# Kernel tuning notes

Measured on AMD Instinct MI355X. Metric: run time of the kernel, lower is better.

## Reference

```python
import jax, jax.numpy as jnp
import numpy as np

K = 20
EPS = 1e-5

def _knn(x, k):
    # x: (B,C,N); returns indices of k nearest neighbors (incl. self): (B,N,k)
    xx = jnp.sum(x * x, axis=1)                          # (B,N)
    inner = jnp.einsum('bcn,bcm->bnm', x, x)             # (B,N,N)
    neg_d = 2.0 * inner - xx[:, :, None] - xx[:, None, :]
    return jax.lax.top_k(neg_d, k)[1]

def _graph_feature(x, k):
    # x: (B,C,N) -> (B,2C,N,k) with [x_j - x_i, x_i]
    idx = _knn(x, k)
    xt = jnp.transpose(x, (0, 2, 1))                     # (B,N,C)
    nb = jax.vmap(lambda f, i: f[i])(xt, idx)            # (B,N,k,C)
    ctr = xt[:, :, None, :]
    feat = jnp.concatenate([nb - ctr, jnp.broadcast_to(ctr, nb.shape)], axis=-1)
    return jnp.transpose(feat, (0, 3, 1, 2))

def _edge_block(h, w, g, b, k):
    # EdgeConv: graph feature -> 1x1 conv -> BN(eval, mean0/var1) -> LeakyReLU(0.2) -> max over k
    f = _graph_feature(h, k)
    f = jnp.einsum('oc,bcnk->bonk', w, f)
    f = g[None, :, None, None] * f / np.sqrt(1.0 + EPS) + b[None, :, None, None]
    f = jnp.where(f >= 0, f, 0.2 * f)
    return jnp.max(f, axis=-1)                           # (B,O,N)

def _forward(features_1, features_2, sw1, sg1, sb1, fw1, fg1, fb1, sw2, sg2, sb2, fw2, fg2, fb2, sw3, sg3, sb3, fw3, fg3, fb3, ew, eg, eb, att_w, tn_w, tn_wb, tn_bias, fc1_w, fc1_b, sc_w, sc_b):
    def dgcnn_pass(x):
        xyz = x[:, :3, :]
        sem = x[:, 3:, :]
        x1 = _edge_block(xyz, sw1, sg1, sb1, K)
        x2 = _edge_block(x1, sw2, sg2, sb2, K)
        x3 = _edge_block(x2, sw3, sg3, sb3, K)
        s1 = _edge_block(sem, fw1, fg1, fb1, K)
        s2 = _edge_block(s1, fw2, fg2, fb2, K)
        s3 = _edge_block(s2, fw3, fg3, fb3, K)
        h = jnp.concatenate([x3, s3], axis=1)            # (B,2*F3,N)
        h = jnp.einsum('oc,bcn->bon', ew, h)
        h = eg[None, :, None] * h / np.sqrt(1.0 + EPS) + eb[None, :, None]
        h = jnp.where(h >= 0, h, 0.2 * h)
        return jnp.transpose(h, (0, 2, 1))               # (B,N,F3)

    def attention(emb):
        gc = jnp.tanh(jnp.mean(jnp.einsum('bnf,fg->bng', emb, att_w), axis=1))  # (B,F)
        sc = jax.nn.sigmoid(jnp.einsum('bnf,bf->bn', emb, gc))[:, :, None]      # (B,N,1)
        pooled = jnp.einsum('bnf,bnk->bfk', emb, sc)                            # (B,F,1)
        return pooled, sc

    a1 = dgcnn_pass(features_1)
    a2 = dgcnn_pass(features_2)
    p1, att1 = attention(a1)
    p2, att2 = attention(a2)
    e1 = p1[:, :, 0]
    e2 = p2[:, :, 0]
    # NTN: e1^T W[:,:,t] e2 + V [e1;e2] + b
    scoring = jnp.einsum('bf,fgt,bg->bt', e1, tn_w, e2)
    block = jnp.einsum('tc,bc->bt', tn_wb, jnp.concatenate([e1, e2], axis=1))
    tscores = jax.nn.relu(scoring + block + tn_bias[:, 0][None, :])             # (B,T)
    h = jax.nn.relu(tscores @ fc1_w.T + fc1_b)
    score = jax.nn.sigmoid(h @ sc_w.T + sc_b).reshape(-1)                       # (B,)
    return score, att1, att2


def setup_inputs() -> dict:
    key = jax.random.key(0)
    ks = iter(jax.random.split(key, 40))
    def rn(shape, s=0.05):
        return jax.random.normal(next(ks), shape, dtype=jnp.float32) * s
    F1, F2, F3, T, BN = 64, 64, 128, 16, 16
    d = {}
    d['features_1'] = jax.random.normal(next(ks), (8, 131, 1024), dtype=jnp.float32)
    d['features_2'] = jax.random.normal(next(ks), (8, 131, 1024), dtype=jnp.float32)
    d['sw1'] = rn((F1, 6));        d['sg1'] = jnp.ones((F1,));  d['sb1'] = jnp.zeros((F1,))
    d['fw1'] = rn((F1, 256));      d['fg1'] = jnp.ones((F1,));  d['fb1'] = jnp.zeros((F1,))
    d['sw2'] = rn((F2, 2 * F1));   d['sg2'] = jnp.ones((F2,));  d['sb2'] = jnp.zeros((F2,))
    d['fw2'] = rn((F2, 2 * F1));   d['fg2'] = jnp.ones((F2,));  d['fb2'] = jnp.zeros((F2,))
    d['sw3'] = rn((F3, 2 * F2));   d['sg3'] = jnp.ones((F3,));  d['sb3'] = jnp.zeros((F3,))
    d['fw3'] = rn((F3, 2 * F2));   d['fg3'] = jnp.ones((F3,));  d['fb3'] = jnp.zeros((F3,))
    d['ew']  = rn((F3, 2 * F3));   d['eg']  = jnp.ones((F3,));  d['eb']  = jnp.zeros((F3,))
    d['att_w'] = rn((F3, F3))
    d['tn_w'] = rn((F3, F3, T))
    d['tn_wb'] = rn((T, 2 * F3))
    d['tn_bias'] = rn((T, 1))
    d['fc1_w'] = rn((BN, T));  d['fc1_b'] = jnp.zeros((BN,))
    d['sc_w'] = rn((1, BN));   d['sc_b'] = jnp.zeros((1,))
    return d


def reference(features_1, features_2, sw1, sg1, sb1, fw1, fg1, fb1, sw2, sg2, sb2, fw2, fg2, fb2, sw3, sg3, sb3, fw3, fg3, fb3, ew, eg, eb, att_w, tn_w, tn_wb, tn_bias, fc1_w, fc1_b, sc_w, sc_b):
    return _forward(features_1, features_2, sw1, sg1, sb1, fw1, fg1, fb1, sw2, sg2, sb2, fw2, fg2, fb2, sw3, sg3, sb3, fw3, fg3, fb3, ew, eg, eb, att_w, tn_w, tn_wb, tn_bias, fc1_w, fc1_b, sc_w, sc_b)
```

## Files before the change

kernel.cpp:

```cpp
#include <hip/hip_runtime.h>
#include <math.h>

#define INV_SQRT1P 0.99999500003749968754f

typedef short v8s  __attribute__((ext_vector_type(8)));
typedef float v16f __attribute__((ext_vector_type(16)));

static __device__ __forceinline__ float lrelu(float f){ return f >= 0.0f ? f : 0.2f*f; }

static __device__ __forceinline__ int lanecnt_below(unsigned long long m){
  int c = __builtin_amdgcn_mbcnt_lo((unsigned)m, 0u);
  return __builtin_amdgcn_mbcnt_hi((unsigned)(m >> 32), c);
}

__global__ void k_ext3(const float* __restrict__ f1, const float* __restrict__ f2,
                       float* __restrict__ out){
  int i = blockIdx.x*256 + threadIdx.x;
  int half = 8*3*1024;
  if (i >= 2*half) return;
  const float* f = (i < half) ? f1 : f2;
  int boff = (i < half) ? 0 : 8;
  int ii = (i < half) ? i : i - half;
  int n  = ii & 1023;
  int bc = ii >> 10;
  int c  = bc % 3;
  int b  = bc / 3;
  out[((size_t)(((b+boff)<<10)+n))*3 + c] = f[((size_t)(b*131 + c) << 10) + n];
}

__global__ __launch_bounds__(256) void k_extT(const float* __restrict__ f1,
    const float* __restrict__ f2, float* __restrict__ out){
  __shared__ float T[32][65];
  int bid = blockIdx.x;
  int nt = bid & 15;
  int ct = (bid >> 4) & 3;
  int bb = bid >> 6;
  const float* f = (bb < 8) ? f1 : f2;
  int b = bb & 7;
  int tid = threadIdx.x;
  #pragma unroll
  for (int it=0; it<8; it++){
    int cc = it*4 + (tid >> 6);
    int nn = tid & 63;
    T[cc][nn] = f[((size_t)(b*131 + 3 + ct*32 + cc) << 10) + nt*64 + nn];
  }
  __syncthreads();
  size_t rowb = ((size_t)bb << 10) + nt*64;
  #pragma unroll
  for (int it=0; it<8; it++){
    int nn = it*8 + (tid >> 5);
    int c  = tid & 31;
    out[(rowb + nn)*128 + ct*32 + c] = T[c][nn];
  }
}

__global__ __launch_bounds__(256) void k_pw(const float* __restrict__ X,
    unsigned short* __restrict__ PH, unsigned short* __restrict__ PL,
    float* __restrict__ xxout, const float* __restrict__ Wm,
    unsigned short* __restrict__ PWH, unsigned short* __restrict__ PWL,
    int C, int Kp, int O, int nwblk, int nrowsB, int wsplit, int doxx){
  int nkc = Kp >> 4;
  if ((int)blockIdx.x < nwblk){
    int gid = blockIdx.x*256 + threadIdx.x;
    int nchunk = (nrowsB/32)*nkc;
    if (gid >= nchunk*64) return;
    int lane = gid & 63;
    int chunk = gid >> 6;
    int jb = chunk / nkc, kc = chunk - jb*nkc;
    int j = jb*32 + (lane & 31);
    int k0 = kc*16 + ((lane>>5)<<3);
    unsigned short h[8], lo[8];
    #pragma unroll
    for (int t=0;t<8;t++){
      int k = k0 + t;
      float x = 0.f;
      if (k < C){
        if (wsplit) x = (j < O) ? Wm[(size_t)j*2*C + k] : Wm[(size_t)(j-O)*2*C + C + k];
        else        x = Wm[(size_t)j*C + k];
      }
      unsigned u = __float_as_uint(x);
      unsigned h16 = (u + 0x7fffu + ((u>>16)&1u)) >> 16;
      float hf = __uint_as_float(h16 << 16);
      float lf = x - hf;
      unsigned ul = __float_as_uint(lf);
      unsigned l16 = (ul + 0x7fffu + ((ul>>16)&1u)) >> 16;
      h[t] = (unsigned short)h16; lo[t] = (unsigned short)l16;
    }
    size_t o = (size_t)chunk*512 + lane*8;
    *(v8s*)(PWH + o) = *(v8s*)h;
    *(v8s*)(PWL + o) = *(v8s*)lo;
  } else {
    int gid = (blockIdx.x - nwblk)*256 + threadIdx.x;
    int lane = gid & 63;
    int chunk = gid >> 6;
    int rb = chunk / nkc, kc = chunk - rb*nkc;
    int row = rb*32 + (lane & 31);
    int k0 = kc*16 + ((lane>>5)<<3);
    unsigned short h[8], lo[8];
    const float* Xr = X + (size_t)row*C;
    #pragma unroll
    for (int j=0;j<8;j++){
      int k = k0 + j;
      float x = (k < C) ? Xr[k] : 0.f;
      unsigned u = __float_as_uint(x);
      unsigned h16 = (u + 0x7fffu + ((u>>16)&1u)) >> 16;
      float hf = __uint_as_float(h16 << 16);
      float lf = x - hf;
      unsigned ul = __float_as_uint(lf);
      unsigned l16 = (ul + 0x7fffu + ((ul>>16)&1u)) >> 16;
      h[j] = (unsigned short)h16; lo[j] = (unsigned short)l16;
    }
    size_t o = (size_t)chunk*512 + lane*8;
    *(v8s*)(PH + o) = *(v8s*)h;
    *(v8s*)(PL + o) = *(v8s*)lo;
    if (doxx && kc == 0 && (lane & 32) == 0){
      float s = 0.f;
      for (int c=0;c<C;c++) s += Xr[c]*Xr[c];
      xxout[row] = s;
    }
  }
}

__global__ __launch_bounds__(512) void k_dy(const unsigned short* __restrict__ PH,
    const unsigned short* __restrict__ PL, const unsigned short* __restrict__ PWH,
    const unsigned short* __restrict__ PWL, const float* __restrict__ xx,
    int* __restrict__ idx, float* __restrict__ Y, int Kp, int N, int npair, int nymf){
  __shared__ float Sl[16][1024];
  int wave = threadIdx.x >> 6;
  int l = threadIdx.x & 63;
  int nkc = Kp >> 4;

  if ((int)blockIdx.x < nymf){
    int gw = blockIdx.x*8 + wave;
    int mt = gw / npair;
    int pair = gw - mt*npair;
    int jb0 = pair*2, jb1 = pair*2 + 1;
    size_t ao  = ((size_t)mt*nkc)*512 + l*8;
    size_t b0o = ((size_t)jb0*nkc)*512 + l*8;
    size_t b1o = ((size_t)jb1*nkc)*512 + l*8;
    v16f acc0, acc1;
    #pragma unroll
    for (int i=0;i<16;i++){ acc0[i] = 0.f; acc1[i] = 0.f; }
    for (int kc=0; kc<nkc; kc++){
      v8s Ah  = *(const v8s*)(PH + ao);
      v8s Al  = *(const v8s*)(PL + ao);
      v8s B0h = *(const v8s*)(PWH + b0o);
      v8s B0l = *(const v8s*)(PWL + b0o);
      v8s B1h = *(const v8s*)(PWH + b1o);
      v8s B1l = *(const v8s*)(PWL + b1o);
      acc0 = __builtin_amdgcn_mfma_f32_32x32x16_bf16(Ah, B0h, acc0, 0, 0, 0);
      acc1 = __builtin_amdgcn_mfma_f32_32x32x16_bf16(Ah, B1h, acc1, 0, 0, 0);
      acc0 = __builtin_amdgcn_mfma_f32_32x32x16_bf16(Ah, B0l, acc0, 0, 0, 0);
      acc1 = __builtin_amdgcn_mfma_f32_32x32x16_bf16(Ah, B1l, acc1, 0, 0, 0);
      acc0 = __builtin_amdgcn_mfma_f32_32x32x16_bf16(Al, B0h, acc0, 0, 0, 0);
      acc1 = __builtin_amdgcn_mfma_f32_32x32x16_bf16(Al, B1h, acc1, 0, 0, 0);
      ao += 512; b0o += 512; b1o += 512;
    }
    int rbase = mt*32;
    int c0 = pair*64 + (l & 31), c1 = c0 + 32;
    #pragma unroll
    for (int r=0;r<16;r++){
      int rl_ = (r&3) + ((r>>2)<<3) + ((l>>5)<<2);
      float* dst = Y + (size_t)(rbase + rl_)*N;
      dst[c0] = acc0[r];
      dst[c1] = acc1[r];
    }
    return;
  }

  int t = blockIdx.x - nymf;
  int rb = ((t & 7) << 6) | (t >> 3);
  int batch = rb >> 5;
  const float* xxb = xx + (batch<<10);
  int rbase_local = (rb & 31)*32;

  v16f acc[4];
  #pragma unroll
  for (int i=0;i<4;i++){
    #pragma unroll
    for (int j=0;j<16;j++) acc[i][j] = 0.f;
  }
  #pragma unroll
  for (int pp=0; pp<2; pp++){
    int pair = wave*2 + pp;
    size_t a   = ((size_t)rb*nkc)*512 + l*8;
    size_t b0o = ((size_t)(batch*32 + 2*pair)*nkc)*512 + l*8;
    size_t b1o = b0o + (size_t)nkc*512;
    for (int kc=0; kc<nkc; kc++){
      v8s Ah  = *(const v8s*)(PH + a);
      v8s Al  = *(const v8s*)(PL + a);
      v8s B0h = *(const v8s*)(PH + b0o);
      v8s B0l = *(const v8s*)(PL + b0o);
      v8s B1h = *(const v8s*)(PH + b1o);
      v8s B1l = *(const v8s*)(PL + b1o);
      acc[2*pp]   = __builtin_amdgcn_mfma_f32_32x32x16_bf16(Ah, B0h, acc[2*pp],   0, 0, 0);
      acc[2*pp+1] = __builtin_amdgcn_mfma_f32_32x32x16_bf16(Ah, B1h, acc[2*pp+1], 0, 0, 0);
      acc[2*pp]   = __builtin_amdgcn_mfma_f32_32x32x16_bf16(Ah, B0l, acc[2*pp],   0, 0, 0);
      acc[2*pp+1] = __builtin_amdgcn_mfma_f32_32x32x16_bf16(Ah, B1l, acc[2*pp+1], 0, 0, 0);
      acc[2*pp]   = __builtin_amdgcn_mfma_f32_32x32x16_bf16(Al, B0h, acc[2*pp],   0, 0, 0);
      acc[2*pp+1] = __builtin_amdgcn_mfma_f32_32x32x16_bf16(Al, B1h, acc[2*pp+1], 0, 0, 0);
      a += 512; b0o += 512; b1o += 512;
    }
  }

  #pragma unroll
  for (int h=0; h<2; h++){
    #pragma unroll
    for (int pp=0; pp<2; pp++){
      int pair = wave*2 + pp;
      int c0 = pair*64 + (l & 31), c1 = c0 + 32;
      float xc0 = xxb[c0], xc1 = xxb[c1];
      #pragma unroll
      for (int r = 0; r < 8; r++){
        int rr = h*8 + r;
        int rl = (rr&3) + (((rr>>2)&1)<<3) + ((l>>5)<<2);
        float xr = xxb[rbase_local + h*16 + rl];
        Sl[rl][c0] = 2.f*acc[2*pp][rr]   - xr - xc0;
        Sl[rl][c1] = 2.f*acc[2*pp+1][rr] - xr - xc1;
      }
    }
    __syncthreads();
    {
      int hi = l >> 5;
      int li = l & 31;
      int rloc = wave*2 + hi;
      int grow = rb*32 + h*16 + rloc;
      int out_base = grow*20;
      unsigned long long hm = hi ? 0xFFFFFFFF00000000ull : 0x00000000FFFFFFFFull;

      unsigned kv[32];
      #pragma unroll
      for (int j=0;j<32;j++){
        unsigned u = __float_as_uint(Sl[rloc][li + 32*j]);
        kv[j] = (u & 0x80000000u) ? ~u : (u | 0x80000000u);
      }

      unsigned lmax = kv[0];
      #pragma unroll
      for (int j=1;j<32;j++) lmax = lmax > kv[j] ? lmax : kv[j];

      unsigned tau = 0u;
      #pragma unroll
      for (int bit=31; bit>=0; --bit){
        unsigned cand = tau | (1u << bit);
        unsigned long long M = __ballot(lmax >= cand);
        int c = hi ? __popc((unsigned)(M >> 32)) : __popc((unsigned)M);
        tau = (c >= 20) ? cand : tau;
      }

      unsigned long long* sl = (unsigned long long*)&Sl[rloc][0];
      sl[li] = 0ull; sl[li+32] = 0ull;
      int b2 = 0;
      #pragma unroll
      for (int j=0;j<32;j++){
        bool p = kv[j] >= tau;
        unsigned long long M = __ballot(p) & hm;
        if (p){
          int s = b2 + lanecnt_below(M);
          if (s < 64) sl[s] = ((unsigned long long)kv[j] << 32) | (unsigned)(li + 32*j);
        }
        b2 += __popcll(M);
      }

      if (b2 <= 64){
        unsigned long long pk0 = sl[li], pk1 = sl[li+32];
        unsigned vcur = 0u;
        #pragma unroll
        for (int bit=31; bit>=0; --bit){
          unsigned long long cc = (unsigned long long)(vcur | (1u << bit)) << 32;
          unsigned long long B0 = __ballot(pk0 >= cc);
          unsigned long long B1 = __ballot(pk1 >= cc);
          int clo = __popc((unsigned)B0) + __popc((unsigned)B1);
          int chi = __popc((unsigned)(B0>>32)) + __popc((unsigned)(B1>>32));
          int c = hi ? chi : clo;
          vcur = (c >= 20) ? (vcur | (1u << bit)) : vcur;
        }
        unsigned k0 = (unsigned)(pk0 >> 32), k1 = (unsigned)(pk1 >> 32);
        unsigned long long G0 = __ballot(k0 > vcur) & hm;
        unsigned long long G1 = __ballot(k1 > vcur) & hm;
        int ng0 = __popcll(G0);
        int c1  = ng0 + __popcll(G1);
        if (k0 > vcur) idx[out_base + lanecnt_below(G0)] = (int)(pk0 & 0xffffffffu);
        if (k1 > vcur) idx[out_base + ng0 + lanecnt_below(G1)] = (int)(pk1 & 0xffffffffu);
        unsigned long long E0 = __ballot(k0 == vcur) & hm;
        unsigned long long E1 = __ballot(k1 == vcur) & hm;
        int ne0 = __popcll(E0);
        if (k0 == vcur){ int s = c1 + lanecnt_below(E0); if (s < 20) idx[out_base + s] = (int)(pk0 & 0xffffffffu); }
        if (k1 == vcur){ int s = c1 + ne0 + lanecnt_below(E1); if (s < 20) idx[out_base + s] = (int)(pk1 & 0xffffffffu); }
      } else {
        unsigned cur = 0u;
        #pragma unroll 1
        for (int bit=31; bit>=0; --bit){
          unsigned cand = cur | (1u << bit);
          int lc = 0;
          #pragma unroll
          for (int j=0;j<32;j++) lc += (kv[j] >= cand) ? 1 : 0;
          #pragma unroll
          for (int off=1; off<32; off<<=1) lc += __shfl_xor(lc, off, 64);
          cur = (lc >= 20) ? cand : cur;
        }
        int bse = 0;
        #pragma unroll 1
        for (int j=0;j<32;j++){
          unsigned long long Mg = __ballot(kv[j] > cur) & hm;
          if (kv[j] > cur){ int s = bse + lanecnt_below(Mg); idx[out_base + s] = li + 32*j; }
          bse += __popcll(Mg);
        }
        #pragma unroll 1
        for (int j=0;j<32;j++){
          unsigned long long Me = __ballot(kv[j] == cur) & hm;
          if (kv[j] == cur){ int s = bse + lanecnt_below(Me); if (s < 20) idx[out_base + s] = li + 32*j; }
          bse += __popcll(Me);
          if (bse >= 20) break;
        }
      }
    }
    __syncthreads();
  }
}

__global__ __launch_bounds__(256) void k_emb(const unsigned short* __restrict__ PH,
    const unsigned short* __restrict__ PL, const unsigned short* __restrict__ PWH,
    const unsigned short* __restrict__ PWL, const float* __restrict__ eg,
    const float* __restrict__ eb, float* __restrict__ EMB){
  int w = threadIdx.x >> 6;
  int l = threadIdx.x & 63;
  int gw = blockIdx.x*4 + w;
  int mt = gw >> 1, pair = gw & 1;
  const int nkc = 16;
  size_t ao  = ((size_t)mt*nkc)*512 + l*8;
  size_t b0o = ((size_t)(pair*2)*nkc)*512 + l*8;
  size_t b1o = b0o + (size_t)nkc*512;
  v16f acc0, acc1;
  #pragma unroll
  for (int i=0;i<16;i++){ acc0[i] = 0.f; acc1[i] = 0.f; }
  for (int kc=0; kc<nkc; kc++){
    v8s Ah  = *(const v8s*)(PH + ao);
    v8s Al  = *(const v8s*)(PL + ao);
    v8s B0h = *(const v8s*)(PWH + b0o);
    v8s B0l = *(const v8s*)(PWL + b0o);
    v8s B1h = *(const v8s*)(PWH + b1o);
    v8s B1l = *(const v8s*)(PWL + b1o);
    acc0 = __builtin_amdgcn_mfma_f32_32x32x16_bf16(Ah, B0h, acc0, 0, 0, 0);
    acc1 = __builtin_amdgcn_mfma_f32_32x32x16_bf16(Ah, B1h, acc1, 0, 0, 0);
    acc0 = __builtin_amdgcn_mfma_f32_32x32x16_bf16(Ah, B0l, acc0, 0, 0, 0);
    acc1 = __builtin_amdgcn_mfma_f32_32x32x16_bf16(Ah, B1l, acc1, 0, 0, 0);
    acc0 = __builtin_amdgcn_mfma_f32_32x32x16_bf16(Al, B0h, acc0, 0, 0, 0);
    acc1 = __builtin_amdgcn_mfma_f32_32x32x16_bf16(Al, B1h, acc1, 0, 0, 0);
    ao += 512; b0o += 512; b1o += 512;
  }
  int rbase = mt*32;
  int c0 = pair*64 + (l & 31), c1 = c0 + 32;
  float g0 = eg[c0]*INV_SQRT1P, g1 = eg[c1]*INV_SQRT1P;
  float bb0 = eb[c0], bb1 = eb[c1];
  #pragma unroll
  for (int r=0;r<16;r++){
    int rl_ = (r&3) + ((r>>2)<<3) + ((l>>5)<<2);
    float* dst = EMB + (size_t)(rbase + rl_)*128;
    dst[c0] = lrelu(g0*acc0[r] + bb0);
    dst[c1] = lrelu(g1*acc1[r] + bb1);
  }
}

__global__ __launch_bounds__(256) void k_edge(const float* __restrict__ Y, const int* __restrict__ idx,
    const float* __restrict__ g, const float* __restrict__ bias,
    float* __restrict__ out, int O, int ldo, int ooff){
  int rpb = 256/O;
  int rloc = threadIdx.x/O;
  int o = threadIdx.x - rloc*O;
  int row = blockIdx.x*rpb + rloc;
  int b = row >> 10;
  __shared__ int js[4][20];
  int nj = rpb*20;
  if (threadIdx.x < nj) js[threadIdx.x/20][threadIdx.x%20] = idx[(blockIdx.x*rpb)*20 + threadIdx.x];
  __syncthreads();
  int O2 = O*2;
  float y1c = Y[(size_t)row*O2 + o];
  float d   = Y[(size_t)row*O2 + O + o] - y1c;
  float sc  = g[o] * INV_SQRT1P;
  float bb  = bias[o];
  const float* Yb = Y + ((size_t)(b<<10))*O2;
  float best = -1e38f;
  #pragma unroll
  for (int k=0;k<20;k++){
    float f = sc * (Yb[(size_t)js[rloc][k]*O2 + o] + d) + bb;
    best = fmaxf(best, lrelu(f));
  }
  out[(size_t)row*ldo + ooff + o] = best;
}

__global__ __launch_bounds__(1024) void k_meangc(const float* __restrict__ emb,
     const float* __restrict__ att_w, float* __restrict__ gc){
  int b = blockIdx.x; int f = threadIdx.x & 127; int ny = threadIdx.x >> 7;
  const float* e = emb + ((size_t)(b<<10) + ny*128)*128 + f;
  float s = 0.f;
  for (int n=0;n<128;n++) s += e[n*128];
  __shared__ float red[8][128];
  __shared__ float mr[128];
  red[ny][f] = s;
  __syncthreads();
  if (ny == 0){
    float t = 0.f;
    #pragma unroll
    for (int i=0;i<8;i++) t += red[i][f];
    mr[f] = t * (1.0f/1024.0f);
  }
  __syncthreads();
  if (threadIdx.x < 128){
    int g = threadIdx.x;
    float s2 = 0.f;
    for (int ff=0; ff<128; ff++) s2 += mr[ff]*att_w[ff*128+g];
    gc[b*128+g] = tanhf(s2);
  }
}

__global__ __launch_bounds__(256) void k_sc(const float* __restrict__ emb, const float* __restrict__ gc,
     float* __restrict__ sc, float* __restrict__ attout){
  int wave = threadIdx.x >> 6;
  int l = threadIdx.x & 63;
  int row = blockIdx.x*4 + wave;
  int b = row >> 10;
  const float* e  = emb + (size_t)row*128;
  const float* gb = gc + b*128;
  float p = e[l]*gb[l] + e[l+64]*gb[l+64];
  #pragma unroll
  for (int off=32; off>0; off>>=1) p += __shfl_xor(p, off, 64);
  if (l == 0){
    float s = 1.0f/(1.0f + expf(-p));
    sc[row] = s;
    attout[row] = s;
  }
}

__global__ __launch_bounds__(1024) void k_pool(const float* __restrict__ emb, const float* __restrict__ sc,
     float* __restrict__ ep){
  int b = blockIdx.x; int f = threadIdx.x & 127; int ny = threadIdx.x >> 7;
  const float* e  = emb + ((size_t)(b<<10) + ny*128)*128 + f;
  const float* sb = sc + (b<<10) + ny*128;
  float s = 0.f;
  for (int n=0;n<128;n++) s += e[n*128]*sb[n];
  __shared__ float red[8][128];
  red[ny][f] = s;
  __syncthreads();
  if (ny == 0){
    float t = 0.f;
    #pragma unroll
    for (int i=0;i<8;i++) t += red[i][f];
    ep[b*128+f] = t;
  }
}

__global__ __launch_bounds__(256) void k_tnet(const float* __restrict__ e1, const float* __restrict__ e2,
    const float* __restrict__ tn_w, const float* __restrict__ tn_wb, const float* __restrict__ tn_bias,
    float* __restrict__ tsout){
  int b = blockIdx.x; int t = threadIdx.x; int tt = t & 15; int fs = t >> 4;
  __shared__ float E1[128], E2[128], red[16][17];
  if (t < 128){ E1[t] = e1[b*128+t]; E2[t] = e2[b*128+t]; }
  __syncthreads();
  float acc = 0.f;
  for (int f = fs*8; f < fs*8+8; f++){
    const float* tw = tn_w + f*128*16 + tt;
    float partial = 0.f;
    for (int g=0; g<128; g++) partial += E2[g]*tw[g*16];
    acc += E1[f]*partial;
  }
  red[fs][tt] = acc;
  __syncthreads();
  if (t < 16){
    float s = 0.f;
    #pragma unroll
    for (int i=0;i<16;i++) s += red[i][t];
    float acc2 = 0.f;
    for (int c=0;c<128;c++) acc2 += tn_wb[t*256+c]*E1[c] + tn_wb[t*256+128+c]*E2[c];
    float v = s + acc2 + tn_bias[t];
    tsout[b*16+t] = v > 0.f ? v : 0.f;
  }
}

__global__ __launch_bounds__(128) void k_score2(const float* __restrict__ ts,
   const float* __restrict__ fc1_w, const float* __restrict__ fc1_b,
   const float* __restrict__ sc_w, const float* __restrict__ sc_b, float* __restrict__ out){
  int t = threadIdx.x; int b = t >> 4, i = t & 15;
  __shared__ float h2[8][17];
  float a = 0.f;
  #pragma unroll
  for (int k=0;k<16;k++) a += ts[b*16+k]*fc1_w[i*16+k];
  a += fc1_b[i];
  h2[b][i] = a > 0.f ? a : 0.f;
  __syncthreads();
  if (t < 8){
    float s = 0.f;
    #pragma unroll
    for (int k=0;k<16;k++) s += h2[t][k]*sc_w[k];
    s += sc_b[0];
    out[t] = 1.0f/(1.0f + expf(-s));
  }
}

extern "C" void kernel_launch(void* const* d_in, const int* in_sizes, int n_in,
                              void* d_out, int out_size, void* d_ws, size_t ws_size,
                              hipStream_t stream){
  const float* f1  = (const float*)d_in[0];
  const float* f2  = (const float*)d_in[1];
  const float* sw1 = (const float*)d_in[2];  const float* sg1 = (const float*)d_in[3];  const float* sb1 = (const float*)d_in[4];
  const float* fw1 = (const float*)d_in[5];  const float* fg1 = (const float*)d_in[6];  const float* fb1 = (const float*)d_in[7];
  const float* sw2 = (const float*)d_in[8];  const float* sg2 = (const float*)d_in[9];  const float* sb2 = (const float*)d_in[10];
  const float* fw2 = (const float*)d_in[11]; const float* fg2 = (const float*)d_in[12]; const float* fb2 = (const float*)d_in[13];
  const float* sw3 = (const float*)d_in[14]; const float* sg3 = (const float*)d_in[15]; const float* sb3 = (const float*)d_in[16];
  const float* fw3 = (const float*)d_in[17]; const float* fg3 = (const float*)d_in[18]; const float* fb3 = (const float*)d_in[19];
  const float* ew  = (const float*)d_in[20]; const float* eg  = (const float*)d_in[21]; const float* eb  = (const float*)d_in[22];
  const float* att_w   = (const float*)d_in[23];
  const float* tn_w    = (const float*)d_in[24];
  const float* tn_wb   = (const float*)d_in[25];
  const float* tn_bias = (const float*)d_in[26];
  const float* fc1_w   = (const float*)d_in[27];
  const float* fc1_b   = (const float*)d_in[28];
  const float* sc_w    = (const float*)d_in[29];
  const float* sc_b    = (const float*)d_in[30];

  float* W    = (float*)d_ws;
  float* T0   = W;
  float* T1   = W + 2097152;
  float* X3S3 = W + 4194304;
  float* EMB  = W + 8388608;
  float* xx   = W + 10485760;
  float* gcb  = W + 10504192;
  float* scb  = W + 10506240;
  float* ep   = W + 10522624;
  float* tsb  = W + 10524672;
  int*   idxb = (int*)(W + 10524800);
  unsigned short* PH = (unsigned short*)(W + 10852480);
  unsigned short* PL = (unsigned short*)(W + 11901056);
  unsigned short* PWH = (unsigned short*)(W + 12949632);
  unsigned short* PWL = (unsigned short*)(W + 12966016);
  float* REG  = W + 12982400;
  unsigned short* PH2 = (unsigned short*)(W + 17176704);
  unsigned short* PL2 = (unsigned short*)(W + 19273856);

  (void)ws_size;
  float* out = (float*)d_out;

  auto edge = [&](const float* xin, int C, int O,
                  const float* w, const float* g, const float* bb,
                  float* xout, int ldo, int ooff){
    int Kp = (C + 15) & ~15;
    int nkc = Kp >> 4;
    int npair = 2*O/64;
    int nwblk = ((2*O/32)*nkc*64 + 255)/256;
    int nymf  = 64*npair;
    k_pw<<<nwblk + 128*nkc, 256, 0, stream>>>(xin, PH, PL, xx, w, PWH, PWL,
        C, Kp, O, nwblk, 2*O, 1, 1);
    k_dy<<<nymf + 512, 512, 0, stream>>>(PH, PL, PWH, PWL, xx, idxb, REG, Kp, 2*O, npair, nymf);
    k_edge<<<16384/(256/O), 256, 0, stream>>>(REG, idxb, g, bb, xout, O, ldo, ooff);
  };

  k_ext3<<<(2*8*3*1024+255)/256, 256, 0, stream>>>(f1, f2, T0);
  edge(T0, 3,   64, sw1, sg1, sb1, T1, 64, 0);
  edge(T1, 64,  64, sw2, sg2, sb2, T0, 64, 0);
  edge(T0, 64, 128, sw3, sg3, sb3, X3S3, 256, 0);
  k_extT<<<1024, 256, 0, stream>>>(f1, f2, T0);
  edge(T0, 128, 64, fw1, fg1, fb1, T1, 64, 0);
  edge(T1, 64,  64, fw2, fg2, fb2, T0, 64, 0);
  edge(T0, 64, 128, fw3, fg3, fb3, X3S3, 256, 128);
  {
    int nwblk = ((128/32)*16*64 + 255)/256;
    k_pw<<<nwblk + 128*16, 256, 0, stream>>>(X3S3, PH2, PL2, xx, ew, PWH, PWL,
        256, 256, 128, nwblk, 128, 0, 0);
    k_emb<<<256, 256, 0, stream>>>(PH2, PL2, PWH, PWL, eg, eb, EMB);
  }
  k_meangc<<<16, 1024, 0, stream>>>(EMB, att_w, gcb);
  k_sc<<<4096, 256, 0, stream>>>(EMB, gcb, scb, out + 8);
  k_pool<<<16, 1024, 0, stream>>>(EMB, scb, ep);

  k_tnet<<<8, 256, 0, stream>>>(ep, ep + 1024, tn_w, tn_wb, tn_bias, tsb);
  k_score2<<<1, 128, 0, stream>>>(tsb, fc1_w, fc1_b, sc_w, sc_b, out);
}
```

Measured before the change: 489.1 us.

## Run xyz and semantic EdgeConv branches concurrently in merged kernel launches

The two independent DGCNN branches (xyz and semantic) were run one after another, giving six sequential edge blocks of three kernels each. Each layer pair is now fused into combined launches (k_pw2, k_dy2, k_edge2) that split the grid between the two branches, each with its own workspace buffers. This halves the kernel count for the edge stages and doubles per-launch parallelism to fill the GPU better. It costs more workspace, and the uneven branch sizes can leave the work imbalanced within a grid.

```diff
diff --git a/kernel.cpp b/kernel.cpp
--- a/kernel.cpp
+++ b/kernel.cpp
@@ -54,14 +54,15 @@
   }
 }
 
-__global__ __launch_bounds__(256) void k_pw(const float* __restrict__ X,
-    unsigned short* __restrict__ PH, unsigned short* __restrict__ PL,
-    float* __restrict__ xxout, const float* __restrict__ Wm,
-    unsigned short* __restrict__ PWH, unsigned short* __restrict__ PWL,
+static __device__ __forceinline__ void pw_body(int bid, int tid,
+    const float* __restrict__ X, unsigned short* __restrict__ PH,
+    unsigned short* __restrict__ PL, float* __restrict__ xxout,
+    const float* __restrict__ Wm, unsigned short* __restrict__ PWH,
+    unsigned short* __restrict__ PWL,
     int C, int Kp, int O, int nwblk, int nrowsB, int wsplit, int doxx){
   int nkc = Kp >> 4;
-  if ((int)blockIdx.x < nwblk){
-    int gid = blockIdx.x*256 + threadIdx.x;
+  if (bid < nwblk){
+    int gid = bid*256 + tid;
     int nchunk = (nrowsB/32)*nkc;
     if (gid >= nchunk*64) return;
     int lane = gid & 63;
@@ -90,7 +91,7 @@
     *(v8s*)(PWH + o) = *(v8s*)h;
     *(v8s*)(PWL + o) = *(v8s*)lo;
   } else {
-    int gid = (blockIdx.x - nwblk)*256 + threadIdx.x;
+    int gid = (bid - nwblk)*256 + tid;
     int lane = gid & 63;
     int chunk = gid >> 6;
     int rb = chunk / nkc, kc = chunk - rb*nkc;
@@ -121,54 +122,73 @@
   }
 }
 
-__global__ __launch_bounds__(512) void k_dy(const unsigned short* __restrict__ PH,
-    const unsigned short* __restrict__ PL, const unsigned short* __restrict__ PWH,
-    const unsigned short* __restrict__ PWL, const float* __restrict__ xx,
-    int* __restrict__ idx, float* __restrict__ Y, int Kp, int N, int npair, int nymf){
-  __shared__ float Sl[16][1024];
-  int wave = threadIdx.x >> 6;
-  int l = threadIdx.x & 63;
-  int nkc = Kp >> 4;
-
-  if ((int)blockIdx.x < nymf){
-    int gw = blockIdx.x*8 + wave;
-    int mt = gw / npair;
-    int pair = gw - mt*npair;
-    int jb0 = pair*2, jb1 = pair*2 + 1;
-    size_t ao  = ((size_t)mt*nkc)*512 + l*8;
-    size_t b0o = ((size_t)jb0*nkc)*512 + l*8;
-    size_t b1o = ((size_t)jb1*nkc)*512 + l*8;
-    v16f acc0, acc1;
-    #pragma unroll
-    for (int i=0;i<16;i++){ acc0[i] = 0.f; acc1[i] = 0.f; }
-    for (int kc=0; kc<nkc; kc++){
-      v8s Ah  = *(const v8s*)(PH + ao);
-      v8s Al  = *(const v8s*)(PL + ao);
-      v8s B0h = *(const v8s*)(PWH + b0o);
-      v8s B0l = *(const v8s*)(PWL + b0o);
-      v8s B1h = *(const v8s*)(PWH + b1o);
-      v8s B1l = *(const v8s*)(PWL + b1o);
-      acc0 = __builtin_amdgcn_mfma_f32_32x32x16_bf16(Ah, B0h, acc0, 0, 0, 0);
-      acc1 = __builtin_amdgcn_mfma_f32_32x32x16_bf16(Ah, B1h, acc1, 0, 0, 0);
-      acc0 = __builtin_amdgcn_mfma_f32_32x32x16_bf16(Ah, B0l, acc0, 0, 0, 0);
-      acc1 = __builtin_amdgcn_mfma_f32_32x32x16_bf16(Ah, B1l, acc1, 0, 0, 0);
-      acc0 = __builtin_amdgcn_mfma_f32_32x32x16_bf16(Al, B0h, acc0, 0, 0, 0);
-      acc1 = __builtin_amdgcn_mfma_f32_32x32x16_bf16(Al, B1h, acc1, 0, 0, 0);
-      ao += 512; b0o += 512; b1o += 512;
-    }
-    int rbase = mt*32;
-    int c0 = pair*64 + (l & 31), c1 = c0 + 32;
-    #pragma unroll
-    for (int r=0;r<16;r++){
-      int rl_ = (r&3) + ((r>>2)<<3) + ((l>>5)<<2);
-      float* dst = Y + (size_t)(rbase + rl_)*N;
-      dst[c0] = acc0[r];
-      dst[c1] = acc1[r];
-    }
-    return;
-  }
-
-  int t = blockIdx.x - nymf;
+__global__ __launch_bounds__(256) void k_pw2(
+    const float* __restrict__ XA, unsigned short* __restrict__ PHa,
+    unsigned short* __restrict__ PLa, float* __restrict__ xxA,
+    const float* __restrict__ WA, unsigned short* __restrict__ PWHa,
+    unsigned short* __restrict__ PWLa, int CA, int KpA, int OA, int nwblkA, int nblkA,
+    const float* __restrict__ XB, unsigned short* __restrict__ PHb,
+    unsigned short* __restrict__ PLb, float* __restrict__ xxB,
+    const float* __restrict__ WB, unsigned short* __restrict__ PWHb,
+    unsigned short* __restrict__ PWLb, int CB, int KpB, int OB, int nwblkB){
+  int bid = blockIdx.x;
+  if (bid < nblkA)
+    pw_body(bid, threadIdx.x, XA, PHa, PLa, xxA, WA, PWHa, PWLa, CA, KpA, OA, nwblkA, 2*OA, 1, 1);
+  else
+    pw_body(bid - nblkA, threadIdx.x, XB, PHb, PLb, xxB, WB, PWHb, PWLb, CB, KpB, OB, nwblkB, 2*OB, 1, 1);
+}
+
+__global__ __launch_bounds__(256) void k_pw(const float* __restrict__ X,
+    unsigned short* __restrict__ PH, unsigned short* __restrict__ PL,
+    float* __restrict__ xxout, const float* __restrict__ Wm,
+    unsigned short* __restrict__ PWH, unsigned short* __restrict__ PWL,
+    int C, int Kp, int O, int nwblk, int nrowsB, int wsplit, int doxx){
+  pw_body(blockIdx.x, threadIdx.x, X, PH, PL, xxout, Wm, PWH, PWL,
+          C, Kp, O, nwblk, nrowsB, wsplit, doxx);
+}
+
+static __device__ __forceinline__ void ymf_body(int gw, int l,
+    const unsigned short* __restrict__ PH, const unsigned short* __restrict__ PL,
+    const unsigned short* __restrict__ PWH, const unsigned short* __restrict__ PWL,
+    float* __restrict__ Y, int nkc, int N, int npair){
+  int mt = gw / npair;
+  int pair = gw - mt*npair;
+  int jb0 = pair*2, jb1 = pair*2 + 1;
+  size_t ao  = ((size_t)mt*nkc)*512 + l*8;
+  size_t b0o = ((size_t)jb0*nkc)*512 + l*8;
+  size_t b1o = ((size_t)jb1*nkc)*512 + l*8;
+  v16f acc0, acc1;
+  #pragma unroll
+  for (int i=0;i<16;i++){ acc0[i] = 0.f; acc1[i] = 0.f; }
+  for (int kc=0; kc<nkc; kc++){
+    v8s Ah  = *(const v8s*)(PH + ao);
+    v8s Al  = *(const v8s*)(PL + ao);
+    v8s B0h = *(const v8s*)(PWH + b0o);
+    v8s B0l = *(const v8s*)(PWL + b0o);
+    v8s B1h = *(const v8s*)(PWH + b1o);
+    v8s B1l = *(const v8s*)(PWL + b1o);
+    acc0 = __builtin_amdgcn_mfma_f32_32x32x16_bf16(Ah, B0h, acc0, 0, 0, 0);
+    acc1 = __builtin_amdgcn_mfma_f32_32x32x16_bf16(Ah, B1h, acc1, 0, 0, 0);
+    acc0 = __builtin_amdgcn_mfma_f32_32x32x16_bf16(Ah, B0l, acc0, 0, 0, 0);
+    acc1 = __builtin_amdgcn_mfma_f32_32x32x16_bf16(Ah, B1l, acc1, 0, 0, 0);
+    acc0 = __builtin_amdgcn_mfma_f32_32x32x16_bf16(Al, B0h, acc0, 0, 0, 0);
+    acc1 = __builtin_amdgcn_mfma_f32_32x32x16_bf16(Al, B1h, acc1, 0, 0, 0);
+    ao += 512; b0o += 512; b1o += 512;
+  }
+  int rbase = mt*32;
+  int c0 = pair*64 + (l & 31), c1 = c0 + 32;
+  #pragma unroll
+  for (int r=0;r<16;r++){
+    int rl_ = (r&3) + ((r>>2)<<3) + ((l>>5)<<2);
+    float* dst = Y + (size_t)(rbase + rl_)*N;
+    dst[c0] = acc0[r];
+    dst[c1] = acc1[r];
+  }
+}
+
+static __device__ void dtk_body(float (&Sl)[16][1024], int t, int wave, int l,
+    const unsigned short* __restrict__ PH, const unsigned short* __restrict__ PL,
+    const float* __restrict__ xx, int* __restrict__ idx, int nkc){
   int rb = ((t & 7) << 6) | (t >> 3);
   int batch = rb >> 5;
   const float* xxb = xx + (batch<<10);
@@ -319,6 +339,34 @@
   }
 }
 
+__global__ __launch_bounds__(512) void k_dy2(
+    const unsigned short* __restrict__ PHa, const unsigned short* __restrict__ PLa,
+    const unsigned short* __restrict__ PWHa, const unsigned short* __restrict__ PWLa,
+    const float* __restrict__ xxA, int* __restrict__ idxA, float* __restrict__ Ya,
+    int KpA, int NA, int npairA, int nymfA,
+    const unsigned short* __restrict__ PHb, const unsigned short* __restrict__ PLb,
+    const unsigned short* __restrict__ PWHb, const unsigned short* __restrict__ PWLb,
+    const float* __restrict__ xxB, int* __restrict__ idxB, float* __restrict__ Yb,
+    int KpB, int NB, int npairB, int nymfB){
+  __shared__ float Sl[16][1024];
+  int wave = threadIdx.x >> 6;
+  int l = threadIdx.x & 63;
+  int bid = (int)blockIdx.x;
+  int nblkA = nymfA + 512;
+  if (bid < nblkA){
+    if (bid < nymfA)
+      ymf_body(bid*8 + wave, l, PHa, PLa, PWHa, PWLa, Ya, KpA >> 4, NA, npairA);
+    else
+      dtk_body(Sl, bid - nymfA, wave, l, PHa, PLa, xxA, idxA, KpA >> 4);
+  } else {
+    int b2 = bid - nblkA;
+    if (b2 < nymfB)
+      ymf_body(b2*8 + wave, l, PHb, PLb, PWHb, PWLb, Yb, KpB >> 4, NB, npairB);
+    else
+      dtk_body(Sl, b2 - nymfB, wave, l, PHb, PLb, xxB, idxB, KpB >> 4);
+  }
+}
+
 __global__ __launch_bounds__(256) void k_emb(const unsigned short* __restrict__ PH,
     const unsigned short* __restrict__ PL, const unsigned short* __restrict__ PWH,
     const unsigned short* __restrict__ PWL, const float* __restrict__ eg,
@@ -362,17 +410,17 @@
   }
 }
 
-__global__ __launch_bounds__(256) void k_edge(const float* __restrict__ Y, const int* __restrict__ idx,
+static __device__ void edge_body(int bid, int tid, int (&js)[4][20],
+    const float* __restrict__ Y, const int* __restrict__ idx,
     const float* __restrict__ g, const float* __restrict__ bias,
     float* __restrict__ out, int O, int ldo, int ooff){
   int rpb = 256/O;
-  int rloc = threadIdx.x/O;
-  int o = threadIdx.x - rloc*O;
-  int row = blockIdx.x*rpb + rloc;
+  int rloc = tid/O;
+  int o = tid - rloc*O;
+  int row = bid*rpb + rloc;
   int b = row >> 10;
-  __shared__ int js[4][20];
   int nj = rpb*20;
-  if (threadIdx.x < nj) js[threadIdx.x/20][threadIdx.x%20] = idx[(blockIdx.x*rpb)*20 + threadIdx.x];
+  if (tid < nj) js[tid/20][tid%20] = idx[(bid*rpb)*20 + tid];
   __syncthreads();
   int O2 = O*2;
   float y1c = Y[(size_t)row*O2 + o];
@@ -387,6 +435,21 @@
     best = fmaxf(best, lrelu(f));
   }
   out[(size_t)row*ldo + ooff + o] = best;
+}
+
+__global__ __launch_bounds__(256) void k_edge2(
+    const float* __restrict__ Ya, const int* __restrict__ idxA,
+    const float* __restrict__ gA, const float* __restrict__ bA,
+    float* __restrict__ outA, int OA, int ldoA, int ooffA, int ngridA,
+    const float* __restrict__ Yb, const int* __restrict__ idxB,
+    const float* __restrict__ gB, const float* __restrict__ bB,
+    float* __restrict__ outB, int OB, int ldoB, int ooffB){
+  __shared__ int js[4][20];
+  int bid = (int)blockIdx.x;
+  if (bid < ngridA)
+    edge_body(bid, threadIdx.x, js, Ya, idxA, gA, bA, outA, OA, ldoA, ooffA);
+  else
+    edge_body(bid - ngridA, threadIdx.x, js, Yb, idxB, gB, bB, outB, OB, ldoB, ooffB);
 }
 
 __global__ __launch_bounds__(1024) void k_meangc(const float* __restrict__ emb,
@@ -519,54 +582,74 @@
   const float* sc_b    = (const float*)d_in[30];
 
   float* W    = (float*)d_ws;
-  float* T0   = W;
-  float* T1   = W + 2097152;
-  float* X3S3 = W + 4194304;
-  float* EMB  = W + 8388608;
-  float* xx   = W + 10485760;
-  float* gcb  = W + 10504192;
-  float* scb  = W + 10506240;
-  float* ep   = W + 10522624;
-  float* tsb  = W + 10524672;
-  int*   idxb = (int*)(W + 10524800);
-  unsigned short* PH = (unsigned short*)(W + 10852480);
-  unsigned short* PL = (unsigned short*)(W + 11901056);
-  unsigned short* PWH = (unsigned short*)(W + 12949632);
-  unsigned short* PWL = (unsigned short*)(W + 12966016);
-  float* REG  = W + 12982400;
-  unsigned short* PH2 = (unsigned short*)(W + 17176704);
-  unsigned short* PL2 = (unsigned short*)(W + 19273856);
+  float* Tx0  = W;
+  float* Tx1  = W + 1048576;
+  float* Ts0  = W + 2097152;
+  float* Ts1  = W + 4194304;
+  float* X3S3 = W + 5242880;
+  float* EMB  = W + 9437184;
+  float* xxA  = W + 11534336;
+  float* xxB  = W + 11550720;
+  float* gcb  = W + 11567104;
+  float* scb  = W + 11569152;
+  float* ep   = W + 11585536;
+  float* tsb  = W + 11587584;
+  int*   idxA = (int*)(W + 11587712);
+  int*   idxB = (int*)(W + 11915392);
+  unsigned short* PHa  = (unsigned short*)(W + 12243072);
+  unsigned short* PLa  = (unsigned short*)(W + 13291648);
+  unsigned short* PHb  = (unsigned short*)(W + 14340224);
+  unsigned short* PLb  = (unsigned short*)(W + 15388800);
+  unsigned short* PWHa = (unsigned short*)(W + 16437376);
+  unsigned short* PWLa = (unsigned short*)(W + 16453760);
+  unsigned short* PWHb = (unsigned short*)(W + 16470144);
+  unsigned short* PWLb = (unsigned short*)(W + 16486528);
+  float* REGa = W + 16502912;
+  float* REGb = W + 20697216;
+  unsigned short* PH2 = (unsigned short*)(W + 24891520);
+  unsigned short* PL2 = (unsigned short*)(W + 26988672);
 
   (void)ws_size;
   float* out = (float*)d_out;
 
-  auto edge = [&](const float* xin, int C, int O,
-                  const float* w, const float* g, const float* bb,
-                  float* xout, int ldo, int ooff){
-    int Kp = (C + 15) & ~15;
-    int nkc = Kp >> 4;
-    int npair = 2*O/64;
-    int nwblk = ((2*O/32)*nkc*64 + 255)/256;
-    int nymf  = 64*npair;
-    k_pw<<<nwblk + 128*nkc, 256, 0, stream>>>(xin, PH, PL, xx, w, PWH, PWL,
-        C, Kp, O, nwblk, 2*O, 1, 1);
-    k_dy<<<nymf + 512, 512, 0, stream>>>(PH, PL, PWH, PWL, xx, idxb, REG, Kp, 2*O, npair, nymf);
-    k_edge<<<16384/(256/O), 256, 0, stream>>>(REG, idxb, g, bb, xout, O, ldo, ooff);
+  auto edge2 = [&](const float* xa, int CA, int OA, const float* wa,
+                   const float* ga, const float* ba, float* xoutA, int ldoA, int ooffA,
+                   const float* xb, int CB, int OB, const float* wb,
+                   const float* gb, const float* bb, float* xoutB, int ldoB, int ooffB){
+    int KpA = (CA + 15) & ~15, KpB = (CB + 15) & ~15;
+    int nkcA = KpA >> 4,       nkcB = KpB >> 4;
+    int npairA = 2*OA/64,      npairB = 2*OB/64;
+    int nwblkA = ((2*OA/32)*nkcA*64 + 255)/256;
+    int nwblkB = ((2*OB/32)*nkcB*64 + 255)/256;
+    int nblkA  = nwblkA + 128*nkcA;
+    int nblkB  = nwblkB + 128*nkcB;
+    int nymfA  = 64*npairA, nymfB = 64*npairB;
+    k_pw2<<<nblkA + nblkB, 256, 0, stream>>>(
+        xa, PHa, PLa, xxA, wa, PWHa, PWLa, CA, KpA, OA, nwblkA, nblkA,
+        xb, PHb, PLb, xxB, wb, PWHb, PWLb, CB, KpB, OB, nwblkB);
+    k_dy2<<<(nymfA + 512) + (nymfB + 512), 512, 0, stream>>>(
+        PHa, PLa, PWHa, PWLa, xxA, idxA, REGa, KpA, 2*OA, npairA, nymfA,
+        PHb, PLb, PWHb, PWLb, xxB, idxB, REGb, KpB, 2*OB, npairB, nymfB);
+    int ngridA = 16384/(256/OA);
+    int ngridB = 16384/(256/OB);
+    k_edge2<<<ngridA + ngridB, 256, 0, stream>>>(
+        REGa, idxA, ga, ba, xoutA, OA, ldoA, ooffA, ngridA,
+        REGb, idxB, gb, bb, xoutB, OB, ldoB, ooffB);
   };
 
-  k_ext3<<<(2*8*3*1024+255)/256, 256, 0, stream>>>(f1, f2, T0);
-  edge(T0, 3,   64, sw1, sg1, sb1, T1, 64, 0);
-  edge(T1, 64,  64, sw2, sg2, sb2, T0, 64, 0);
-  edge(T0, 64, 128, sw3, sg3, sb3, X3S3, 256, 0);
-  k_extT<<<1024, 256, 0, stream>>>(f1, f2, T0);
-  edge(T0, 128, 64, fw1, fg1, fb1, T1, 64, 0);
-  edge(T1, 64,  64, fw2, fg2, fb2, T0, 64, 0);
-  edge(T0, 64, 128, fw3, fg3, fb3, X3S3, 256, 128);
+  k_ext3<<<(2*8*3*1024+255)/256, 256, 0, stream>>>(f1, f2, Tx0);
+  k_extT<<<1024, 256, 0, stream>>>(f1, f2, Ts0);
+  edge2(Tx0, 3,   64, sw1, sg1, sb1, Tx1, 64, 0,
+        Ts0, 128, 64, fw1, fg1, fb1, Ts1, 64, 0);
+  edge2(Tx1, 64,  64, sw2, sg2, sb2, Tx0, 64, 0,
+        Ts1, 64,  64, fw2, fg2, fb2, Ts0, 64, 0);
+  edge2(Tx0, 64, 128, sw3, sg3, sb3, X3S3, 256, 0,
+        Ts0, 64, 128, fw3, fg3, fb3, X3S3, 256, 128);
   {
     int nwblk = ((128/32)*16*64 + 255)/256;
-    k_pw<<<nwblk + 128*16, 256, 0, stream>>>(X3S3, PH2, PL2, xx, ew, PWH, PWL,
+    k_pw<<<nwblk + 128*16, 256, 0, stream>>>(X3S3, PH2, PL2, xxA, ew, PWHa, PWLa,
         256, 256, 128, nwblk, 128, 0, 0);
-    k_emb<<<256, 256, 0, stream>>>(PH2, PL2, PWH, PWL, eg, eb, EMB);
+    k_emb<<<256, 256, 0, stream>>>(PH2, PL2, PWHa, PWLa, eg, eb, EMB);
   }
   k_meangc<<<16, 1024, 0, stream>>>(EMB, att_w, gcb);
   k_sc<<<4096, 256, 0, stream>>>(EMB, gcb, scb, out + 8);
```

New measurement: 574.0 us. 17.3% more time.
